# Optimization experiments

Measured on AMD Instinct MI355X. Metric: run time of the kernel, lower is better.

Reference implementation:

```python
import jax, jax.numpy as jnp
import numpy as np

WIN = 5          # ssim_window_size
SIGMA = 1.5      # Gaussian sigma used by the reference implementation
C1 = 0.01 ** 2
C2 = 0.03 ** 2
MS_WEIGHTS = jnp.array([0.0448, 0.2856, 0.3001, 0.2363, 0.1333], dtype=jnp.float32)


def make_window(num_channel, dtype):
    x = jnp.arange(WIN, dtype=jnp.float32) - (WIN // 2)
    g = jnp.exp(-(x ** 2) / (2.0 * SIGMA ** 2))
    g = g / g.sum()
    w2 = jnp.outer(g, g)
    return jnp.broadcast_to(w2, (num_channel, 1, WIN, WIN)).astype(dtype)


def dwconv(x, w):
    pad = WIN // 2
    return jax.lax.conv_general_dilated(
        x, w, window_strides=(1, 1), padding=[(pad, pad), (pad, pad)],
        dimension_numbers=('NCHW', 'OIHW', 'NCHW'),
        feature_group_count=x.shape[1])


def compute_ssim(img1, img2):
    w = make_window(img1.shape[1], img1.dtype)
    mu1 = dwconv(img1, w)
    mu2 = dwconv(img2, w)
    mu1_sq = mu1 * mu1
    mu2_sq = mu2 * mu2
    mu1_mu2 = mu1 * mu2
    sigma1_sq = dwconv(img1 * img1, w) - mu1_sq
    sigma2_sq = dwconv(img2 * img2, w) - mu2_sq
    sigma12 = dwconv(img1 * img2, w) - mu1_mu2
    ssim_map = ((2 * mu1_mu2 + C1) * (2 * sigma12 + C2)) / (
        (mu1_sq + mu2_sq + C1) * (sigma1_sq + sigma2_sq + C2))
    cs = jnp.mean((2.0 * sigma12 + C2) / (sigma1_sq + sigma2_sq + C2))
    return jnp.mean(ssim_map), cs


def avg_pool2(x):
    s = jax.lax.reduce_window(x, jnp.array(0, x.dtype), jax.lax.add,
                              (1, 1, 2, 2), (1, 1, 2, 2), 'VALID')
    return s / jnp.array(4, x.dtype)


def ms_ssim(img1, img2):
    levels = MS_WEIGHTS.shape[0]
    ssims, mcs = [], []
    for _ in range(levels):
        s, cs = compute_ssim(img1, img2)
        ssims.append(s)
        mcs.append(cs)
        img1 = avg_pool2(img1)
        img2 = avg_pool2(img2)
    ssims = (jnp.stack(ssims) + 1) / 2
    mcs = (jnp.stack(mcs) + 1) / 2
    pow1 = mcs ** MS_WEIGHTS
    pow2 = ssims ** MS_WEIGHTS
    return jnp.prod(pow1[:-1] * pow2[-1])


def setup_inputs() -> dict:
    key = jax.random.key(0)
    k1, k2 = jax.random.split(key)
    shape = (32, 3, 512, 512)
    img1 = jax.random.uniform(k1, shape, dtype=jnp.float32)
    img2 = jax.random.uniform(k2, shape, dtype=jnp.float32)
    return {"img1": img1, "img2": img2}


def reference(img1, img2):
    return ms_ssim(img1, img2)
```

## Files before the change

### kernel.cpp

```cpp
#include <hip/hip_runtime.h>
#include <math.h>


typedef float f2 __attribute__((ext_vector_type(2)));

#if __has_builtin(__builtin_elementwise_fma)
static __device__ __forceinline__ f2 vfma(f2 a, f2 b, f2 c) {
    return __builtin_elementwise_fma(a, b, c);
}
#else
static __device__ __forceinline__ f2 vfma(f2 a, f2 b, f2 c) {
    f2 d; d.x = __builtin_fmaf(a.x, b.x, c.x); d.y = __builtin_fmaf(a.y, b.y, c.y);
    return d;
}
#endif

#define C1F 0.0001f
#define C2F 0.0009f
#define GW0f 0.12007838f
#define GW1f 0.23388060f
#define GW2f 0.29208204f

#define HCONV(DST, VL, V01, VR) do { \
    const f2 t1_ = (VL) + (VR); \
    f2 mid_; mid_.x = (VL).y + (V01).y; mid_.y = (V01).x + (VR).x; \
    (DST) = vfma(G1v, mid_, vfma(G0v, t1_, G2v * (V01))); \
} while (0)

#define VCONV(OUT, WN, S0,S1,S2,S3,S4) do { \
    const f2 t_ = WN[S0] + WN[S4]; \
    const f2 u_ = WN[S1] + WN[S3]; \
    (OUT) = vfma(G1v, u_, vfma(G0v, t_, G2v * WN[S2])); \
} while (0)

#define ROW(J,S0,S1,S2,S3,S4) do { \
    const int i = i0 + (J); \
    if (i < iters) { \
        const int r = y0 + i - 2; \
        const int rc = min(max(r, 0), H - 1); \
        const float rvf = ((unsigned)r < (unsigned)H) ? 1.f : 0.f; \
        const f2 mVv = {rvf, rvf}; \
        const f2 mLV = mL * mVv; \
        const f2 mRV = mR * mVv; \
        const float* r1_ = p1 + (size_t)rc * (size_t)W; \
        const float* r2_ = p2 + (size_t)rc * (size_t)W; \
        const f2 XL  = *(const f2*)(r1_ + offL) * mLV; \
        const f2 X01 = *(const f2*)(r1_ + offC) * mVv; \
        const f2 XR  = *(const f2*)(r1_ + offR) * mRV; \
        const f2 ZL  = *(const f2*)(r2_ + offL) * mLV; \
        const f2 Z01 = *(const f2*)(r2_ + offC) * mVv; \
        const f2 ZR  = *(const f2*)(r2_ + offR) * mRV; \
        const f2 QL = vfma(ZL,  ZL,  XL  * XL); \
        const f2 QC = vfma(Z01, Z01, X01 * X01); \
        const f2 QR = vfma(ZR,  ZR,  XR  * XR); \
        const f2 PL = XL  * ZL; \
        const f2 PC = X01 * Z01; \
        const f2 PR = XR  * ZR; \
        HCONV(wa[(J)], XL, X01, XR); \
        HCONV(wb[(J)], ZL, Z01, ZR); \
        HCONV(wq[(J)], QL, QC,  QR); \
        HCONV(wp[(J)], PL, PC,  PR); \
        if (i >= 4) { \
            f2 Av, Bv, Qv, Pv; \
            VCONV(Av, wa, S0,S1,S2,S3,S4); \
            VCONV(Bv, wb, S0,S1,S2,S3,S4); \
            VCONV(Qv, wq, S0,S1,S2,S3,S4); \
            VCONV(Pv, wp, S0,S1,S2,S3,S4); \
            const f2 ABv   = Av * Bv; \
            const f2 A2B2v = vfma(Bv, Bv, Av * Av); \
            const f2 S12v  = vfma(TWOv, Pv - ABv, C2v); \
            const f2 SDENv = (Qv - A2B2v) + C2v; \
            const f2 D1v   = A2B2v + C1v; \
            const f2 N1v   = vfma(TWOv, ABv, C1v); \
            const f2 DENv  = D1v * SDENv; \
            f2 RDv; \
            RDv.x = __builtin_amdgcn_rcpf(DENv.x); \
            RDv.y = __builtin_amdgcn_rcpf(DENv.y); \
            const f2 SSv = N1v * S12v * RDv; \
            const f2 CCv = S12v * D1v * RDv; \
            if (gC) { ACCS += SSv; ACCC += CCv; } \
        } \
        if (q1 && (i & 1) && i >= 3 && i <= TROWS + 1 && gC) { \
            const f2 sx_ = X01 + PX; \
            const f2 sz_ = Z01 + PZ; \
            const size_t po_ = (size_t)(r >> 1) * WP + (c0 >> 1); \
            q1[po_] = (sx_.x + sx_.y) * 0.25f; \
            q2[po_] = (sz_.x + sz_.y) * 0.25f; \
        } \
        PX = X01; PZ = Z01; \
    } \
} while (0)

template<int TROWS, int WPB>
__global__ __launch_bounds__(WPB * 64)
void ssim_level_kernel(const float* __restrict__ img1,
                       const float* __restrict__ img2,
                       int H, int W, int SX, int SY,
                       float* __restrict__ pool1,
                       float* __restrict__ pool2,
                       double* __restrict__ block_out)
{
    const int lane = threadIdx.x & 63;
    const int wv   = threadIdx.x >> 6;
    const int w    = blockIdx.x * WPB + wv;

    const int spp   = SX * SY;
    const int plane = w / spp;
    const int rem   = w - plane * spp;
    const int sy    = rem / SX;
    const int sx    = rem - sy * SX;

    const int base = sx * 128;
    const int y0   = sy * TROWS;
    const int c0   = base + 2 * lane;
    const bool gC = (unsigned)c0 < (unsigned)W;
    const bool gL = (c0 - 2) >= 0 && (c0 - 2) < W;
    const bool gR = (c0 + 2) < W;
    const int offL = gL ? (c0 - 2) : 0;
    const int offC = gC ? c0 : 0;
    const int offR = gR ? (c0 + 2) : 0;
    const f2 mL = {gL ? 1.f : 0.f, gL ? 1.f : 0.f};
    const f2 mR = {gR ? 1.f : 0.f, gR ? 1.f : 0.f};

    const float* p1 = img1 + (size_t)plane * H * W;
    const float* p2 = img2 + (size_t)plane * H * W;
    const int WP = W >> 1;
    float* q1 = pool1 ? pool1 + (size_t)plane * (H >> 1) * WP : nullptr;
    float* q2 = pool2 ? pool2 + (size_t)plane * (H >> 1) * WP : nullptr;

    const f2 G0v  = {GW0f, GW0f};
    const f2 G1v  = {GW1f, GW1f};
    const f2 G2v  = {GW2f, GW2f};
    const f2 C1v  = {C1F, C1F};
    const f2 C2v  = {C2F, C2F};
    const f2 TWOv = {2.f, 2.f};

    f2 wa[5], wb[5], wq[5], wp[5];
    f2 PX = {0.f, 0.f}, PZ = {0.f, 0.f};
    f2 ACCS = {0.f, 0.f}, ACCC = {0.f, 0.f};

    const int iters = TROWS + 4;
    #pragma unroll
    for (int i0 = 0; i0 < iters; i0 += 5) {
        ROW(0, 1, 2, 3, 4, 0);
        ROW(1, 2, 3, 4, 0, 1);
        ROW(2, 3, 4, 0, 1, 2);
        ROW(3, 4, 0, 1, 2, 3);
        ROW(4, 0, 1, 2, 3, 4);
    }

    float accs = ACCS.x + ACCS.y;
    float accc = ACCC.x + ACCC.y;
    #pragma unroll
    for (int o = 32; o > 0; o >>= 1) {
        accs += __shfl_down(accs, o, 64);
        accc += __shfl_down(accc, o, 64);
    }

    __shared__ double sred[WPB][2];
    if (lane == 0) { sred[wv][0] = (double)accs; sred[wv][1] = (double)accc; }
    __syncthreads();
    if (threadIdx.x == 0) {
        double s = 0.0, c = 0.0;
        #pragma unroll
        for (int k = 0; k < WPB; ++k) { s += sred[k][0]; c += sred[k][1]; }
        block_out[2 * (size_t)blockIdx.x]     = s;
        block_out[2 * (size_t)blockIdx.x + 1] = c;
    }
}

static constexpr int NBLK[5] = {3072, 768, 384, 384, 192};
static constexpr int BOFF[5] = {0, 3072, 3840, 4224, 4608};

__global__ __launch_bounds__(1024)
void ssim_final_kernel(const double* __restrict__ bsum, float* __restrict__ out)
{
    __shared__ double partial[16][2];
    __shared__ double lvl[5][2];
    const double npx[5] = {96.0*512*512, 96.0*256*256, 96.0*128*128,
                           96.0*64*64,   96.0*32*32};
    const int tid = threadIdx.x, lane = tid & 63, wv = tid >> 6;

    for (int l = 0; l < 5; ++l) {
        double s = 0.0, c = 0.0;
        for (int k = tid; k < NBLK[l]; k += 1024) {
            s += bsum[2 * (size_t)(BOFF[l] + k)];
            c += bsum[2 * (size_t)(BOFF[l] + k) + 1];
        }
        #pragma unroll
        for (int o = 32; o > 0; o >>= 1) {
            s += __shfl_down(s, o, 64);
            c += __shfl_down(c, o, 64);
        }
        if (lane == 0) { partial[wv][0] = s; partial[wv][1] = c; }
        __syncthreads();
        if (tid == 0) {
            double ts = 0.0, tc = 0.0;
            for (int k = 0; k < 16; ++k) { ts += partial[k][0]; tc += partial[k][1]; }
            lvl[l][0] = ts / npx[l];
            lvl[l][1] = tc / npx[l];
        }
        __syncthreads();
    }
    if (tid == 0) {
        const double wgt[5] = {0.0448, 0.2856, 0.3001, 0.2363, 0.1333};
        double ssim4 = (lvl[4][0] + 1.0) * 0.5;
        double P = pow(ssim4, wgt[4]);
        double r = pow((lvl[0][1] + 1.0) * 0.5, wgt[0]) *
                   pow((lvl[1][1] + 1.0) * 0.5, wgt[1]) *
                   pow((lvl[2][1] + 1.0) * 0.5, wgt[2]) *
                   pow((lvl[3][1] + 1.0) * 0.5, wgt[3]);
        r *= P * P * P * P;
        out[0] = (float)r;
    }
}

extern "C" void kernel_launch(void* const* d_in, const int* in_sizes, int n_in,
                              void* d_out, int out_size, void* d_ws, size_t ws_size,
                              hipStream_t stream)
{
    const float* img1 = (const float*)d_in[0];
    const float* img2 = (const float*)d_in[1];
    float* out = (float*)d_out;

    char* ws = (char*)d_ws;
    double* wsum = (double*)ws;
    size_t off = 262144;
    const size_t P = 96;
    float* l1a = (float*)(ws + off); off += P * 256 * 256 * sizeof(float);
    float* l1b = (float*)(ws + off); off += P * 256 * 256 * sizeof(float);
    float* l2a = (float*)(ws + off); off += P * 128 * 128 * sizeof(float);
    float* l2b = (float*)(ws + off); off += P * 128 * 128 * sizeof(float);
    float* l3a = (float*)(ws + off); off += P * 64 * 64 * sizeof(float);
    float* l3b = (float*)(ws + off); off += P * 64 * 64 * sizeof(float);
    float* l4a = (float*)(ws + off); off += P * 32 * 32 * sizeof(float);
    float* l4b = (float*)(ws + off); off += P * 32 * 32 * sizeof(float);

    ssim_level_kernel<16, 4><<<3072, 256, 0, stream>>>(
        img1, img2, 512, 512, 4, 32, l1a, l1b, wsum + 2 * (size_t)BOFF[0]);
    ssim_level_kernel<16, 4><<<768, 256, 0, stream>>>(
        l1a, l1b, 256, 256, 2, 16, l2a, l2b, wsum + 2 * (size_t)BOFF[1]);
    ssim_level_kernel<8, 4><<<384, 256, 0, stream>>>(
        l2a, l2b, 128, 128, 1, 16, l3a, l3b, wsum + 2 * (size_t)BOFF[2]);
    ssim_level_kernel<4, 4><<<384, 256, 0, stream>>>(
        l3a, l3b, 64, 64, 1, 16, l4a, l4b, wsum + 2 * (size_t)BOFF[3]);
    ssim_level_kernel<4, 4><<<192, 256, 0, stream>>>(
        l4a, l4b, 32, 32, 1, 8, nullptr, nullptr, wsum + 2 * (size_t)BOFF[4]);

    ssim_final_kernel<<<1, 1024, 0, stream>>>(wsum, out);
}
```

Baseline: 291.1 us.

## Prefetch next input row into double-buffered registers and templatize image dimensions

Each row-step now issues the global loads for the next row into a second register set before computing the current row, so load latency overlaps with the convolution arithmetic. The ring-buffer slot indexing is adjusted and the unroll widened to 10 steps so the ping-pong buffers line up. Image height, width and the tile counts become template constants, which removes runtime divisions and index arithmetic, and launch bounds now request occupancy 4. The extra live registers for the prefetch buffers may raise register pressure and lower occupancy.

```diff
diff --git a/kernel.cpp b/kernel.cpp
--- a/kernel.cpp
+++ b/kernel.cpp
@@ -33,33 +33,46 @@
     (OUT) = vfma(G1v, u_, vfma(G0v, t_, G2v * WN[S2])); \
 } while (0)
 
-#define ROW(J,S0,S1,S2,S3,S4) do { \
+#define LOADROW(I, PB) do { \
+    if ((I) < ITERS) { \
+        const int r_ = y0 + (I) - 2; \
+        const int rc_ = min(max(r_, 0), H - 1); \
+        const float rvf_ = ((unsigned)r_ < (unsigned)H) ? 1.f : 0.f; \
+        mV##PB.x = rvf_; mV##PB.y = rvf_; \
+        const float* r1_ = p1 + (size_t)rc_ * W; \
+        const float* r2_ = p2 + (size_t)rc_ * W; \
+        XL##PB = *(const f2*)(r1_ + offL); \
+        XC##PB = *(const f2*)(r1_ + offC); \
+        XR##PB = *(const f2*)(r1_ + offR); \
+        ZL##PB = *(const f2*)(r2_ + offL); \
+        ZC##PB = *(const f2*)(r2_ + offC); \
+        ZR##PB = *(const f2*)(r2_ + offR); \
+    } \
+} while (0)
+
+#define STEP(J,S0,S1,S2,S3,S4,PB,PN) do { \
     const int i = i0 + (J); \
-    if (i < iters) { \
-        const int r = y0 + i - 2; \
-        const int rc = min(max(r, 0), H - 1); \
-        const float rvf = ((unsigned)r < (unsigned)H) ? 1.f : 0.f; \
-        const f2 mVv = {rvf, rvf}; \
+    if (i < ITERS) { \
+        LOADROW(i + 1, PN); \
+        const f2 mVv = mV##PB; \
         const f2 mLV = mL * mVv; \
         const f2 mRV = mR * mVv; \
-        const float* r1_ = p1 + (size_t)rc * (size_t)W; \
-        const float* r2_ = p2 + (size_t)rc * (size_t)W; \
-        const f2 XL  = *(const f2*)(r1_ + offL) * mLV; \
-        const f2 X01 = *(const f2*)(r1_ + offC) * mVv; \
-        const f2 XR  = *(const f2*)(r1_ + offR) * mRV; \
-        const f2 ZL  = *(const f2*)(r2_ + offL) * mLV; \
-        const f2 Z01 = *(const f2*)(r2_ + offC) * mVv; \
-        const f2 ZR  = *(const f2*)(r2_ + offR) * mRV; \
-        const f2 QL = vfma(ZL,  ZL,  XL  * XL); \
+        const f2 XLv = XL##PB * mLV; \
+        const f2 X01 = XC##PB * mVv; \
+        const f2 XRv = XR##PB * mRV; \
+        const f2 ZLv = ZL##PB * mLV; \
+        const f2 Z01 = ZC##PB * mVv; \
+        const f2 ZRv = ZR##PB * mRV; \
+        const f2 QL = vfma(ZLv, ZLv, XLv * XLv); \
         const f2 QC = vfma(Z01, Z01, X01 * X01); \
-        const f2 QR = vfma(ZR,  ZR,  XR  * XR); \
-        const f2 PL = XL  * ZL; \
+        const f2 QR = vfma(ZRv, ZRv, XRv * XRv); \
+        const f2 PL = XLv * ZLv; \
         const f2 PC = X01 * Z01; \
-        const f2 PR = XR  * ZR; \
-        HCONV(wa[(J)], XL, X01, XR); \
-        HCONV(wb[(J)], ZL, Z01, ZR); \
-        HCONV(wq[(J)], QL, QC,  QR); \
-        HCONV(wp[(J)], PL, PC,  PR); \
+        const f2 PR = XRv * ZRv; \
+        HCONV(wa[(S4)], XLv, X01, XRv); \
+        HCONV(wb[(S4)], ZLv, Z01, ZRv); \
+        HCONV(wq[(S4)], QL,  QC,  QR); \
+        HCONV(wp[(S4)], PL,  PC,  PR); \
         if (i >= 4) { \
             f2 Av, Bv, Qv, Pv; \
             VCONV(Av, wa, S0,S1,S2,S3,S4); \
@@ -83,7 +96,7 @@
         if (q1 && (i & 1) && i >= 3 && i <= TROWS + 1 && gC) { \
             const f2 sx_ = X01 + PX; \
             const f2 sz_ = Z01 + PZ; \
-            const size_t po_ = (size_t)(r >> 1) * WP + (c0 >> 1); \
+            const size_t po_ = (size_t)((y0 + i - 2) >> 1) * WP + (c0 >> 1); \
             q1[po_] = (sx_.x + sx_.y) * 0.25f; \
             q2[po_] = (sz_.x + sz_.y) * 0.25f; \
         } \
@@ -91,20 +104,24 @@
     } \
 } while (0)
 
-template<int TROWS, int WPB>
-__global__ __launch_bounds__(WPB * 64)
+template<int TROWS, int WPB, int H, int W>
+__global__ __launch_bounds__(WPB * 64, 4)
 void ssim_level_kernel(const float* __restrict__ img1,
                        const float* __restrict__ img2,
-                       int H, int W, int SX, int SY,
                        float* __restrict__ pool1,
                        float* __restrict__ pool2,
                        double* __restrict__ block_out)
 {
+    constexpr int SX = (W + 127) / 128;
+    constexpr int SY = H / TROWS;
+    constexpr int spp = SX * SY;
+    constexpr int ITERS = TROWS + 4;
+    constexpr int WP = W >> 1;
+
     const int lane = threadIdx.x & 63;
     const int wv   = threadIdx.x >> 6;
     const int w    = blockIdx.x * WPB + wv;
 
-    const int spp   = SX * SY;
     const int plane = w / spp;
     const int rem   = w - plane * spp;
     const int sy    = rem / SX;
@@ -124,7 +141,6 @@
 
     const float* p1 = img1 + (size_t)plane * H * W;
     const float* p2 = img2 + (size_t)plane * H * W;
-    const int WP = W >> 1;
     float* q1 = pool1 ? pool1 + (size_t)plane * (H >> 1) * WP : nullptr;
     float* q2 = pool2 ? pool2 + (size_t)plane * (H >> 1) * WP : nullptr;
 
@@ -139,14 +155,22 @@
     f2 PX = {0.f, 0.f}, PZ = {0.f, 0.f};
     f2 ACCS = {0.f, 0.f}, ACCC = {0.f, 0.f};
 
-    const int iters = TROWS + 4;
+    f2 XL0, XC0, XR0, ZL0, ZC0, ZR0, mV0;
+    f2 XL1, XC1, XR1, ZL1, ZC1, ZR1, mV1;
+
+    LOADROW(0, 0);
     #pragma unroll
-    for (int i0 = 0; i0 < iters; i0 += 5) {
-        ROW(0, 1, 2, 3, 4, 0);
-        ROW(1, 2, 3, 4, 0, 1);
-        ROW(2, 3, 4, 0, 1, 2);
-        ROW(3, 4, 0, 1, 2, 3);
-        ROW(4, 0, 1, 2, 3, 4);
+    for (int i0 = 0; i0 < ITERS; i0 += 10) {
+        STEP(0, 1, 2, 3, 4, 0, 0, 1);
+        STEP(1, 2, 3, 4, 0, 1, 1, 0);
+        STEP(2, 3, 4, 0, 1, 2, 0, 1);
+        STEP(3, 4, 0, 1, 2, 3, 1, 0);
+        STEP(4, 0, 1, 2, 3, 4, 0, 1);
+        STEP(5, 1, 2, 3, 4, 0, 1, 0);
+        STEP(6, 2, 3, 4, 0, 1, 0, 1);
+        STEP(7, 3, 4, 0, 1, 2, 1, 0);
+        STEP(8, 4, 0, 1, 2, 3, 0, 1);
+        STEP(9, 0, 1, 2, 3, 4, 1, 0);
     }
 
     float accs = ACCS.x + ACCS.y;
@@ -236,16 +260,16 @@
     float* l4a = (float*)(ws + off); off += P * 32 * 32 * sizeof(float);
     float* l4b = (float*)(ws + off); off += P * 32 * 32 * sizeof(float);
 
-    ssim_level_kernel<16, 4><<<3072, 256, 0, stream>>>(
-        img1, img2, 512, 512, 4, 32, l1a, l1b, wsum + 2 * (size_t)BOFF[0]);
-    ssim_level_kernel<16, 4><<<768, 256, 0, stream>>>(
-        l1a, l1b, 256, 256, 2, 16, l2a, l2b, wsum + 2 * (size_t)BOFF[1]);
-    ssim_level_kernel<8, 4><<<384, 256, 0, stream>>>(
-        l2a, l2b, 128, 128, 1, 16, l3a, l3b, wsum + 2 * (size_t)BOFF[2]);
-    ssim_level_kernel<4, 4><<<384, 256, 0, stream>>>(
-        l3a, l3b, 64, 64, 1, 16, l4a, l4b, wsum + 2 * (size_t)BOFF[3]);
-    ssim_level_kernel<4, 4><<<192, 256, 0, stream>>>(
-        l4a, l4b, 32, 32, 1, 8, nullptr, nullptr, wsum + 2 * (size_t)BOFF[4]);
+    ssim_level_kernel<16, 4, 512, 512><<<3072, 256, 0, stream>>>(
+        img1, img2, l1a, l1b, wsum + 2 * (size_t)BOFF[0]);
+    ssim_level_kernel<16, 4, 256, 256><<<768, 256, 0, stream>>>(
+        l1a, l1b, l2a, l2b, wsum + 2 * (size_t)BOFF[1]);
+    ssim_level_kernel<8, 4, 128, 128><<<384, 256, 0, stream>>>(
+        l2a, l2b, l3a, l3b, wsum + 2 * (size_t)BOFF[2]);
+    ssim_level_kernel<4, 4, 64, 64><<<384, 256, 0, stream>>>(
+        l3a, l3b, l4a, l4b, wsum + 2 * (size_t)BOFF[3]);
+    ssim_level_kernel<4, 4, 32, 32><<<192, 256, 0, stream>>>(
+        l4a, l4b, nullptr, nullptr, wsum + 2 * (size_t)BOFF[4]);
 
     ssim_final_kernel<<<1, 1024, 0, stream>>>(wsum, out);
 }
```

Result: no change. 293.1 us (+0.7%).

## Vertical-first separable conv with float4 loads and shuffle-based horizontal halo

Applied to the files above, without the earlier changes.

Restructures the SSIM level kernel so each lane loads one float4 per row per image and runs the vertical 5-tap pass first, computing squares and products per tap on the fly. The horizontal pass then pulls neighbour columns from adjacent lanes with wave shuffles instead of issuing overlapping left/right halo loads. Strips overlap by two columns, with ownership masks so no pixel is counted twice. Dimensions become template constants and the coarse levels use single-row tiles with more blocks. This is meant to cut redundant global loads and use wider memory transactions, at the cost of extra shuffle instructions, extra FMAs from the per-tap squaring, and some redundant halo columns.

```diff
diff --git a/kernel.cpp b/kernel.cpp
--- a/kernel.cpp
+++ b/kernel.cpp
@@ -3,17 +3,14 @@
 
 
 typedef float f2 __attribute__((ext_vector_type(2)));
-
-#if __has_builtin(__builtin_elementwise_fma)
-static __device__ __forceinline__ f2 vfma(f2 a, f2 b, f2 c) {
+typedef float f4 __attribute__((ext_vector_type(4)));
+
+static __device__ __forceinline__ f2 vfma2(f2 a, f2 b, f2 c) {
     return __builtin_elementwise_fma(a, b, c);
 }
-#else
-static __device__ __forceinline__ f2 vfma(f2 a, f2 b, f2 c) {
-    f2 d; d.x = __builtin_fmaf(a.x, b.x, c.x); d.y = __builtin_fmaf(a.y, b.y, c.y);
-    return d;
-}
-#endif
+static __device__ __forceinline__ f4 vfma4(f4 a, f4 b, f4 c) {
+    return __builtin_elementwise_fma(a, b, c);
+}
 
 #define C1F 0.0001f
 #define C2F 0.0009f
@@ -21,136 +18,188 @@
 #define GW1f 0.23388060f
 #define GW2f 0.29208204f
 
+#define VCONV4(OUT, WN, S0,S1,S2,S3,S4) do { \
+    const f4 t_ = WN[S0] + WN[S4]; \
+    const f4 u_ = WN[S1] + WN[S3]; \
+    (OUT) = vfma4(u_, G1q, vfma4(t_, G0q, WN[S2] * G2q)); \
+} while (0)
+
+#define VQCONV4(OUT, WX, WZ, S0,S1,S2,S3,S4) do { \
+    f4 t1_ = vfma4(WX[S0], WX[S0], WX[S4] * WX[S4]); \
+    t1_ = vfma4(WZ[S0], WZ[S0], t1_); t1_ = vfma4(WZ[S4], WZ[S4], t1_); \
+    f4 t2_ = vfma4(WX[S1], WX[S1], WX[S3] * WX[S3]); \
+    t2_ = vfma4(WZ[S1], WZ[S1], t2_); t2_ = vfma4(WZ[S3], WZ[S3], t2_); \
+    const f4 t3_ = vfma4(WZ[S2], WZ[S2], WX[S2] * WX[S2]); \
+    (OUT) = vfma4(t2_, G1q, vfma4(t1_, G0q, t3_ * G2q)); \
+} while (0)
+
+#define VPCONV4(OUT, WX, WZ, S0,S1,S2,S3,S4) do { \
+    const f4 t1_ = vfma4(WX[S0], WZ[S0], WX[S4] * WZ[S4]); \
+    const f4 t2_ = vfma4(WX[S1], WZ[S1], WX[S3] * WZ[S3]); \
+    const f4 t3_ = WX[S2] * WZ[S2]; \
+    (OUT) = vfma4(t2_, G1q, vfma4(t1_, G0q, t3_ * G2q)); \
+} while (0)
+
 #define HCONV(DST, VL, V01, VR) do { \
     const f2 t1_ = (VL) + (VR); \
     f2 mid_; mid_.x = (VL).y + (V01).y; mid_.y = (V01).x + (VR).x; \
-    (DST) = vfma(G1v, mid_, vfma(G0v, t1_, G2v * (V01))); \
-} while (0)
-
-#define VCONV(OUT, WN, S0,S1,S2,S3,S4) do { \
-    const f2 t_ = WN[S0] + WN[S4]; \
-    const f2 u_ = WN[S1] + WN[S3]; \
-    (OUT) = vfma(G1v, u_, vfma(G0v, t_, G2v * WN[S2])); \
-} while (0)
-
-#define ROW(J,S0,S1,S2,S3,S4) do { \
-    const int i = i0 + (J); \
-    if (i < iters) { \
-        const int r = y0 + i - 2; \
-        const int rc = min(max(r, 0), H - 1); \
-        const float rvf = ((unsigned)r < (unsigned)H) ? 1.f : 0.f; \
-        const f2 mVv = {rvf, rvf}; \
-        const f2 mLV = mL * mVv; \
-        const f2 mRV = mR * mVv; \
-        const float* r1_ = p1 + (size_t)rc * (size_t)W; \
-        const float* r2_ = p2 + (size_t)rc * (size_t)W; \
-        const f2 XL  = *(const f2*)(r1_ + offL) * mLV; \
-        const f2 X01 = *(const f2*)(r1_ + offC) * mVv; \
-        const f2 XR  = *(const f2*)(r1_ + offR) * mRV; \
-        const f2 ZL  = *(const f2*)(r2_ + offL) * mLV; \
-        const f2 Z01 = *(const f2*)(r2_ + offC) * mVv; \
-        const f2 ZR  = *(const f2*)(r2_ + offR) * mRV; \
-        const f2 QL = vfma(ZL,  ZL,  XL  * XL); \
-        const f2 QC = vfma(Z01, Z01, X01 * X01); \
-        const f2 QR = vfma(ZR,  ZR,  XR  * XR); \
-        const f2 PL = XL  * ZL; \
-        const f2 PC = X01 * Z01; \
-        const f2 PR = XR  * ZR; \
-        HCONV(wa[(J)], XL, X01, XR); \
-        HCONV(wb[(J)], ZL, Z01, ZR); \
-        HCONV(wq[(J)], QL, QC,  QR); \
-        HCONV(wp[(J)], PL, PC,  PR); \
-        if (i >= 4) { \
-            f2 Av, Bv, Qv, Pv; \
-            VCONV(Av, wa, S0,S1,S2,S3,S4); \
-            VCONV(Bv, wb, S0,S1,S2,S3,S4); \
-            VCONV(Qv, wq, S0,S1,S2,S3,S4); \
-            VCONV(Pv, wp, S0,S1,S2,S3,S4); \
-            const f2 ABv   = Av * Bv; \
-            const f2 A2B2v = vfma(Bv, Bv, Av * Av); \
-            const f2 S12v  = vfma(TWOv, Pv - ABv, C2v); \
-            const f2 SDENv = (Qv - A2B2v) + C2v; \
-            const f2 D1v   = A2B2v + C1v; \
-            const f2 N1v   = vfma(TWOv, ABv, C1v); \
-            const f2 DENv  = D1v * SDENv; \
-            f2 RDv; \
-            RDv.x = __builtin_amdgcn_rcpf(DENv.x); \
-            RDv.y = __builtin_amdgcn_rcpf(DENv.y); \
-            const f2 SSv = N1v * S12v * RDv; \
-            const f2 CCv = S12v * D1v * RDv; \
-            if (gC) { ACCS += SSv; ACCC += CCv; } \
+    (DST) = vfma2(mid_, G1p, vfma2(t1_, G0p, (V01) * G2p)); \
+} while (0)
+
+#define SSIM_PX2(A,B,Q,P, SS, CC) do { \
+    const f2 ab_ = (A) * (B); \
+    const f2 a2b2_ = vfma2((B), (B), (A) * (A)); \
+    const f2 s12_ = vfma2(TWOp, (P) - ab_, C2p); \
+    const f2 sden_ = ((Q) - a2b2_) + C2p; \
+    const f2 d1_ = a2b2_ + C1p; \
+    const f2 n1_ = vfma2(TWOp, ab_, C1p); \
+    const f2 den_ = d1_ * sden_; \
+    f2 rd_; \
+    rd_.x = __builtin_amdgcn_rcpf(den_.x); \
+    rd_.y = __builtin_amdgcn_rcpf(den_.y); \
+    (SS) = n1_ * s12_ * rd_; \
+    (CC) = s12_ * d1_ * rd_; \
+} while (0)
+
+#define STEP(I, S0,S1,S2,S3,S4) do { \
+    const int r_in = y0 + (I) - 2; \
+    const int rc_ = min(max(r_in, 0), H - 1); \
+    const float rv_ = ((unsigned)r_in < (unsigned)H) ? 1.f : 0.f; \
+    const f4 m_ = mE * rv_; \
+    wx[S4] = *(const f4*)(p1 + (size_t)rc_ * W + lc) * m_; \
+    wz[S4] = *(const f4*)(p2 + (size_t)rc_ * W + lc) * m_; \
+    if ((I) >= 4) { \
+        f4 vx, vz, vq, vp; \
+        VCONV4(vx, wx, S0,S1,S2,S3,S4); \
+        VCONV4(vz, wz, S0,S1,S2,S3,S4); \
+        VQCONV4(vq, wx, wz, S0,S1,S2,S3,S4); \
+        VPCONV4(vp, wx, wz, S0,S1,S2,S3,S4); \
+        f2 ux, uz, uq, up, dx, dz, dq, dp; \
+        ux.x = __shfl_up(vx.z, 1);   ux.y = __shfl_up(vx.w, 1); \
+        uz.x = __shfl_up(vz.z, 1);   uz.y = __shfl_up(vz.w, 1); \
+        uq.x = __shfl_up(vq.z, 1);   uq.y = __shfl_up(vq.w, 1); \
+        up.x = __shfl_up(vp.z, 1);   up.y = __shfl_up(vp.w, 1); \
+        dx.x = __shfl_down(vx.x, 1); dx.y = __shfl_down(vx.y, 1); \
+        dz.x = __shfl_down(vz.x, 1); dz.y = __shfl_down(vz.y, 1); \
+        dq.x = __shfl_down(vq.x, 1); dq.y = __shfl_down(vq.y, 1); \
+        dp.x = __shfl_down(vp.x, 1); dp.y = __shfl_down(vp.y, 1); \
+        ux *= upM; uz *= upM; uq *= upM; up *= upM; \
+        const f2 vxa = vx.xy, vxb = vx.zw; \
+        const f2 vza = vz.xy, vzb = vz.zw; \
+        const f2 vqa = vq.xy, vqb = vq.zw; \
+        const f2 vpa = vp.xy, vpb = vp.zw; \
+        f2 A0, A1, B0, B1, Q0, Q1, P0, P1; \
+        HCONV(A0, ux, vxa, vxb);  HCONV(A1, vxa, vxb, dx); \
+        HCONV(B0, uz, vza, vzb);  HCONV(B1, vza, vzb, dz); \
+        HCONV(Q0, uq, vqa, vqb);  HCONV(Q1, vqa, vqb, dq); \
+        HCONV(P0, up, vpa, vpb);  HCONV(P1, vpa, vpb, dp); \
+        f2 ss_, cc_; \
+        SSIM_PX2(A0, B0, Q0, P0, ss_, cc_); \
+        ACCS0 += ss_ * mO01;  ACCC0 += cc_ * mO01; \
+        SSIM_PX2(A1, B1, Q1, P1, ss_, cc_); \
+        ACCS1 += ss_ * mO23;  ACCC1 += cc_ * mO23; \
+    } \
+    { \
+        const bool pc_ = (TROWS == 1) ? ((I) == 2 && (y0 & 1)) \
+                         : (((I) & 1) && (I) >= 3 && (I) <= TROWS + 1); \
+        if (q1 && pc_) { \
+            const f4 tx_ = wx[S4] + wx[S3]; \
+            const f4 tz_ = wz[S4] + wz[S3]; \
+            const size_t po_ = (size_t)(r_in >> 1) * WP + (c0 >> 1); \
+            if (pOwn0) { q1[po_]   = (tx_.x + tx_.y) * 0.25f; \
+                         q2[po_]   = (tz_.x + tz_.y) * 0.25f; } \
+            if (pOwn2) { q1[po_+1] = (tx_.z + tx_.w) * 0.25f; \
+                         q2[po_+1] = (tz_.z + tz_.w) * 0.25f; } \
         } \
-        if (q1 && (i & 1) && i >= 3 && i <= TROWS + 1 && gC) { \
-            const f2 sx_ = X01 + PX; \
-            const f2 sz_ = Z01 + PZ; \
-            const size_t po_ = (size_t)(r >> 1) * WP + (c0 >> 1); \
-            q1[po_] = (sx_.x + sx_.y) * 0.25f; \
-            q2[po_] = (sz_.x + sz_.y) * 0.25f; \
-        } \
-        PX = X01; PZ = Z01; \
     } \
 } while (0)
 
-template<int TROWS, int WPB>
-__global__ __launch_bounds__(WPB * 64)
+#define BATCH5(T) do { \
+    STEP((T)*5+0, 1,2,3,4,0); \
+    STEP((T)*5+1, 2,3,4,0,1); \
+    STEP((T)*5+2, 3,4,0,1,2); \
+    STEP((T)*5+3, 4,0,1,2,3); \
+    STEP((T)*5+4, 0,1,2,3,4); \
+} while (0)
+
+template<int TROWS, int WPB, int H, int W, int SX>
+__global__ __launch_bounds__(WPB * 64, 3)
 void ssim_level_kernel(const float* __restrict__ img1,
                        const float* __restrict__ img2,
-                       int H, int W, int SX, int SY,
                        float* __restrict__ pool1,
                        float* __restrict__ pool2,
                        double* __restrict__ block_out)
 {
+    constexpr int SY = H / TROWS;
+    constexpr int spp = SX * SY;
+    constexpr int ITERS = TROWS + 4;
+    constexpr int NB = ITERS / 5;
+    static_assert(ITERS % 5 == 0, "TROWS+4 must be divisible by 5");
+    static_assert(NB == 1 || NB == 4, "written for NB in {1,4}");
+    constexpr int WP = W >> 1;
+
     const int lane = threadIdx.x & 63;
     const int wv   = threadIdx.x >> 6;
     const int w    = blockIdx.x * WPB + wv;
 
-    const int spp   = SX * SY;
     const int plane = w / spp;
     const int rem   = w - plane * spp;
     const int sy    = rem / SX;
     const int sx    = rem - sy * SX;
 
-    const int base = sx * 128;
+    const int base = sx * 252;
     const int y0   = sy * TROWS;
-    const int c0   = base + 2 * lane;
-    const bool gC = (unsigned)c0 < (unsigned)W;
-    const bool gL = (c0 - 2) >= 0 && (c0 - 2) < W;
-    const bool gR = (c0 + 2) < W;
-    const int offL = gL ? (c0 - 2) : 0;
-    const int offC = gC ? c0 : 0;
-    const int offR = gR ? (c0 + 2) : 0;
-    const f2 mL = {gL ? 1.f : 0.f, gL ? 1.f : 0.f};
-    const f2 mR = {gR ? 1.f : 0.f, gR ? 1.f : 0.f};
-
-    const float* p1 = img1 + (size_t)plane * H * W;
-    const float* p2 = img2 + (size_t)plane * H * W;
-    const int WP = W >> 1;
+    const int c0   = base + 4 * lane;
+    const int lc   = min(c0, W - 4);
+    const bool lastStrip = (sx == SX - 1);
+
+    f4 mE;
+    mE.x = (c0 + 0 < W) ? 1.f : 0.f;
+    mE.y = (c0 + 1 < W) ? 1.f : 0.f;
+    mE.z = (c0 + 2 < W) ? 1.f : 0.f;
+    mE.w = (c0 + 3 < W) ? 1.f : 0.f;
+    float oOK[4];
+    #pragma unroll
+    for (int j = 0; j < 4; ++j) {
+        const int cj = c0 + j;
+        const bool own = (cj < W) &&
+                         (base == 0 || cj >= base + 2) &&
+                         (cj <= base + 253 || lastStrip);
+        oOK[j] = own ? 1.f : 0.f;
+    }
+    f2 mO01; mO01.x = oOK[0]; mO01.y = oOK[1];
+    f2 mO23; mO23.x = oOK[2]; mO23.y = oOK[3];
+    const bool pOwn0 = (oOK[0] != 0.f) && (oOK[1] != 0.f);
+    const bool pOwn2 = (oOK[2] != 0.f) && (oOK[3] != 0.f);
+    const float upM = (lane == 0 && base == 0) ? 0.f : 1.f;
+
+    const float* p1 = img1 + (size_t)plane * (H * W);
+    const float* p2 = img2 + (size_t)plane * (H * W);
     float* q1 = pool1 ? pool1 + (size_t)plane * (H >> 1) * WP : nullptr;
     float* q2 = pool2 ? pool2 + (size_t)plane * (H >> 1) * WP : nullptr;
 
-    const f2 G0v  = {GW0f, GW0f};
-    const f2 G1v  = {GW1f, GW1f};
-    const f2 G2v  = {GW2f, GW2f};
-    const f2 C1v  = {C1F, C1F};
-    const f2 C2v  = {C2F, C2F};
-    const f2 TWOv = {2.f, 2.f};
-
-    f2 wa[5], wb[5], wq[5], wp[5];
-    f2 PX = {0.f, 0.f}, PZ = {0.f, 0.f};
-    f2 ACCS = {0.f, 0.f}, ACCC = {0.f, 0.f};
-
-    const int iters = TROWS + 4;
-    #pragma unroll
-    for (int i0 = 0; i0 < iters; i0 += 5) {
-        ROW(0, 1, 2, 3, 4, 0);
-        ROW(1, 2, 3, 4, 0, 1);
-        ROW(2, 3, 4, 0, 1, 2);
-        ROW(3, 4, 0, 1, 2, 3);
-        ROW(4, 0, 1, 2, 3, 4);
-    }
-
-    float accs = ACCS.x + ACCS.y;
-    float accc = ACCC.x + ACCC.y;
+    const f4 G0q = {GW0f, GW0f, GW0f, GW0f};
+    const f4 G1q = {GW1f, GW1f, GW1f, GW1f};
+    const f4 G2q = {GW2f, GW2f, GW2f, GW2f};
+    const f2 G0p = {GW0f, GW0f};
+    const f2 G1p = {GW1f, GW1f};
+    const f2 G2p = {GW2f, GW2f};
+    const f2 C1p = {C1F, C1F};
+    const f2 C2p = {C2F, C2F};
+    const f2 TWOp = {2.f, 2.f};
+
+    f4 wx[5], wz[5];
+    f2 ACCS0 = {0.f,0.f}, ACCS1 = {0.f,0.f};
+    f2 ACCC0 = {0.f,0.f}, ACCC1 = {0.f,0.f};
+
+    if constexpr (NB == 4) {
+        BATCH5(0); BATCH5(1); BATCH5(2); BATCH5(3);
+    } else {
+        BATCH5(0);
+    }
+
+    float accs = ACCS0.x + ACCS0.y + ACCS1.x + ACCS1.y;
+    float accc = ACCC0.x + ACCC0.y + ACCC1.x + ACCC1.y;
     #pragma unroll
     for (int o = 32; o > 0; o >>= 1) {
         accs += __shfl_down(accs, o, 64);
@@ -169,8 +218,8 @@
     }
 }
 
-static constexpr int NBLK[5] = {3072, 768, 384, 384, 192};
-static constexpr int BOFF[5] = {0, 3072, 3840, 4224, 4608};
+static constexpr int NBLK[5] = {2304, 768, 3072, 1536, 768};
+static constexpr int BOFF[5] = {0, 2304, 3072, 6144, 7680};
 
 __global__ __launch_bounds__(1024)
 void ssim_final_kernel(const double* __restrict__ bsum, float* __restrict__ out)
@@ -225,7 +274,7 @@
 
     char* ws = (char*)d_ws;
     double* wsum = (double*)ws;
-    size_t off = 262144;
+    size_t off = 524288;
     const size_t P = 96;
     float* l1a = (float*)(ws + off); off += P * 256 * 256 * sizeof(float);
     float* l1b = (float*)(ws + off); off += P * 256 * 256 * sizeof(float);
@@ -236,16 +285,16 @@
     float* l4a = (float*)(ws + off); off += P * 32 * 32 * sizeof(float);
     float* l4b = (float*)(ws + off); off += P * 32 * 32 * sizeof(float);
 
-    ssim_level_kernel<16, 4><<<3072, 256, 0, stream>>>(
-        img1, img2, 512, 512, 4, 32, l1a, l1b, wsum + 2 * (size_t)BOFF[0]);
-    ssim_level_kernel<16, 4><<<768, 256, 0, stream>>>(
-        l1a, l1b, 256, 256, 2, 16, l2a, l2b, wsum + 2 * (size_t)BOFF[1]);
-    ssim_level_kernel<8, 4><<<384, 256, 0, stream>>>(
-        l2a, l2b, 128, 128, 1, 16, l3a, l3b, wsum + 2 * (size_t)BOFF[2]);
-    ssim_level_kernel<4, 4><<<384, 256, 0, stream>>>(
-        l3a, l3b, 64, 64, 1, 16, l4a, l4b, wsum + 2 * (size_t)BOFF[3]);
-    ssim_level_kernel<4, 4><<<192, 256, 0, stream>>>(
-        l4a, l4b, 32, 32, 1, 8, nullptr, nullptr, wsum + 2 * (size_t)BOFF[4]);
+    ssim_level_kernel<16, 4, 512, 512, 3><<<2304, 256, 0, stream>>>(
+        img1, img2, l1a, l1b, wsum + 2 * (size_t)BOFF[0]);
+    ssim_level_kernel<16, 4, 256, 256, 2><<<768, 256, 0, stream>>>(
+        l1a, l1b, l2a, l2b, wsum + 2 * (size_t)BOFF[1]);
+    ssim_level_kernel<1, 4, 128, 128, 1><<<3072, 256, 0, stream>>>(
+        l2a, l2b, l3a, l3b, wsum + 2 * (size_t)BOFF[2]);
+    ssim_level_kernel<1, 4, 64, 64, 1><<<1536, 256, 0, stream>>>(
+        l3a, l3b, l4a, l4b, wsum + 2 * (size_t)BOFF[3]);
+    ssim_level_kernel<1, 4, 32, 32, 1><<<768, 256, 0, stream>>>(
+        l4a, l4b, nullptr, nullptr, wsum + 2 * (size_t)BOFF[4]);
 
     ssim_final_kernel<<<1, 1024, 0, stream>>>(wsum, out);
 }
```

Measured after the change: 778.0 us. +167.3%, slower.
